# Kernel optimization log

Measured on AMD Instinct MI355X. Metric: run time of the kernel, lower is better.

Reference implementation:

```python
import jax, jax.numpy as jnp
import numpy as np
from jax import lax

EPS = 1e-5

def _layernorm(x, w, b):
    m = jnp.mean(x, axis=-1, keepdims=True)
    v = jnp.mean(jnp.square(x - m), axis=-1, keepdims=True)
    return (x - m) * lax.rsqrt(v + EPS) * w + b

def setup_inputs() -> dict:
    D = 2048
    B, S = 4, 4096
    key = jax.random.key(0)
    ks = jax.random.split(key, 16)
    f32 = jnp.float32
    inp = {
        "x": jax.random.normal(ks[0], (B, S, D), f32),
        "norm1_w": jnp.ones((D,), f32), "norm1_b": jnp.zeros((D,), f32),
        "norm2_w": jnp.ones((D,), f32), "norm2_b": jnp.zeros((D,), f32),
        "time_decay": jax.random.normal(ks[1], (D,), f32) * 0.01 - 5.0,
        "time_faaaa": jax.random.normal(ks[2], (D,), f32) * 0.01,
        # Linear weights stored as [in, out]; y = x @ W (equiv to torch x @ W.T)
        "Wr": jax.random.normal(ks[3], (D, D), f32) * 0.02,
        "Wk": jax.random.normal(ks[4], (D, D), f32) * 0.02,
        "Wv": jax.random.normal(ks[5], (D, D), f32) * 0.02,
        "Wo": jax.random.normal(ks[6], (D, D), f32) * 0.02,
        "time_mix_r": jnp.full((1, 1, D), 0.5, f32),
        "time_mix_k": jnp.full((1, 1, D), 0.5, f32),
        "time_mix_v": jnp.full((1, 1, D), 0.5, f32),
        "Wcr": jax.random.normal(ks[7], (D, D), f32) * 0.02,
        "Wck": jax.random.normal(ks[8], (D, 3 * D), f32) * 0.02,
        "Wcv": jax.random.normal(ks[9], (3 * D, D), f32) * 0.02,
        "cm_mix": jnp.full((1, 1, D), 0.5, f32),
    }
    return inp

def _wkv(r, k, v, time_decay, time_faaaa):
    # Elementwise linear recurrence: state_t = state_{t-1} * w + k_t * v_t
    w = jnp.exp(-jnp.exp(time_decay))            # [D]
    r_sig = jax.nn.sigmoid(r)                    # [B,S,D]
    kv = k * v                                   # [B,S,D]
    def step(state, kv_t):
        state = state * w + kv_t
        return state, state
    _, states = lax.scan(step, jnp.zeros_like(kv[:, 0]), jnp.swapaxes(kv, 0, 1))
    states = jnp.swapaxes(states, 0, 1)          # [B,S,D]
    out = r_sig * states
    # bonus only applies at t == 0 in the original loop
    out = out.at[:, 0].add(r_sig[:, 0] * jnp.exp(time_faaaa) * kv[:, 0])
    return out

def reference(x, norm1_w, norm1_b, norm2_w, norm2_b, time_decay, time_faaaa,
              Wr, Wk, Wv, Wo, time_mix_r, time_mix_k, time_mix_v,
              Wcr, Wck, Wcv, cm_mix):
    # time-mixing
    h = _layernorm(x, norm1_w, norm1_b)
    prev = jnp.pad(h[:, :-1], ((0, 0), (1, 0), (0, 0)))
    r = (h * time_mix_r + prev * (1.0 - time_mix_r)) @ Wr
    k = (h * time_mix_k + prev * (1.0 - time_mix_k)) @ Wk
    v = (h * time_mix_v + prev * (1.0 - time_mix_v)) @ Wv
    wkv = _wkv(r, k, v, time_decay, time_faaaa)
    x = x + wkv @ Wo
    # channel-mixing
    h = _layernorm(x, norm2_w, norm2_b)
    prev = jnp.pad(h[:, :-1], ((0, 0), (1, 0), (0, 0)))
    mixed = h * cm_mix + prev * (1.0 - cm_mix)
    r_cm = jax.nn.sigmoid(mixed @ Wcr)
    k_cm = jax.nn.relu(jnp.square(mixed @ Wck))
    x = x + r_cm * (k_cm @ Wcv)
    return x
```

## Files before the change

### kernel.cpp

```cpp
#include <hip/hip_runtime.h>
#include <stdint.h>
#include <stddef.h>


typedef float  f32x4   __attribute__((ext_vector_type(4)));
typedef short  short8  __attribute__((ext_vector_type(8)));
typedef short  short4_ __attribute__((ext_vector_type(4)));
typedef __bf16 bf16x8  __attribute__((ext_vector_type(8)));

constexpr int kD   = 2048;
constexpr int kSeq = 4096;
constexpr int kBat = 4;
constexpr int kM   = kBat * kSeq;
constexpr int kL   = 64;
constexpr int kC   = kSeq / kL;

__device__ __forceinline__ short f2bf(float f) {
  unsigned u = __builtin_bit_cast(unsigned, f);
  u += 0x7FFFu + ((u >> 16) & 1u);
  return (short)(u >> 16);
}
__device__ __forceinline__ float bf2f(short h) {
  unsigned u = ((unsigned)(unsigned short)h) << 16;
  return __builtin_bit_cast(float, u);
}
__device__ __forceinline__ void split_bf(float v, short& hi, short& lo) {
  hi = f2bf(v);
  lo = f2bf(v - bf2f(hi));
}

__device__ __forceinline__ f32x4 block_reduce4(f32x4 v) {
  #pragma unroll
  for (int off = 32; off > 0; off >>= 1) {
    v[0] += __shfl_down(v[0], off);
    v[1] += __shfl_down(v[1], off);
    v[2] += __shfl_down(v[2], off);
    v[3] += __shfl_down(v[3], off);
  }
  __shared__ float sh[4][4];
  const int wid = threadIdx.x >> 6, lane = threadIdx.x & 63;
  if (lane == 0) { sh[wid][0] = v[0]; sh[wid][1] = v[1]; sh[wid][2] = v[2]; sh[wid][3] = v[3]; }
  __syncthreads();
  #pragma unroll
  for (int i = 0; i < 4; ++i) v[i] = sh[0][i] + sh[1][i] + sh[2][i] + sh[3][i];
  return v;
}

__global__ __launch_bounds__(256) void wconvert_kernel(
    const float* __restrict__ W, short* __restrict__ hi, short* __restrict__ lo,
    int K, int N) {
  __shared__ float tile[32][33];
  const int tx = threadIdx.x & 31, ty = threadIdx.x >> 5;
  const int n0 = blockIdx.x * 32, k0 = blockIdx.y * 32;
  #pragma unroll
  for (int i = 0; i < 32; i += 8)
    tile[ty + i][tx] = W[(size_t)(k0 + ty + i) * N + (n0 + tx)];
  __syncthreads();
  #pragma unroll
  for (int i = 0; i < 32; i += 8) {
    float v = tile[tx][ty + i];
    int n = n0 + ty + i, k = k0 + tx;
    short h, l; split_bf(v, h, l);
    hi[(size_t)n * K + k] = h;
    lo[(size_t)n * K + k] = l;
  }
}

__global__ __launch_bounds__(256) void ln1mix_kernel(
    const float* __restrict__ x, const float* __restrict__ w1, const float* __restrict__ b1,
    const float* __restrict__ tmr, const float* __restrict__ tmk, const float* __restrict__ tmv,
    short* __restrict__ mr_hi, short* __restrict__ mr_lo,
    short* __restrict__ mk_hi, short* __restrict__ mk_lo,
    short* __restrict__ mv_hi, short* __restrict__ mv_lo) {
  const int row = blockIdx.x;
  const int s = row & (kSeq - 1);
  const float* xs = x + (size_t)row * kD;
  const int t = threadIdx.x;
  f32x4 a[2];
  f32x4 p[2] = {};
  a[0] = *(const f32x4*)&xs[4 * t];
  a[1] = *(const f32x4*)&xs[1024 + 4 * t];
  if (s > 0) {
    p[0] = *(const f32x4*)&xs[4 * t - kD];
    p[1] = *(const f32x4*)&xs[1024 + 4 * t - kD];
  }
  f32x4 sums = {0.f, 0.f, 0.f, 0.f};
  #pragma unroll
  for (int g = 0; g < 2; ++g)
    #pragma unroll
    for (int j = 0; j < 4; ++j) {
      sums[0] += a[g][j]; sums[1] += a[g][j] * a[g][j];
      sums[2] += p[g][j]; sums[3] += p[g][j] * p[g][j];
    }
  sums = block_reduce4(sums);
  const float inv = 1.f / kD;
  const float ms = sums[0] * inv, vs = sums[1] * inv - ms * ms;
  const float mp = sums[2] * inv, vp = sums[3] * inv - mp * mp;
  const float rs = rsqrtf(vs + 1e-5f);
  const float rp = rsqrtf(vp + 1e-5f);
  #pragma unroll
  for (int g = 0; g < 2; ++g) {
    const int d0 = g * 1024 + 4 * t;
    short4_ rh, rl, kh, kl, vh, vl;
    #pragma unroll
    for (int j = 0; j < 4; ++j) {
      const int d = d0 + j;
      const float w = w1[d], bb = b1[d];
      const float h  = (a[g][j] - ms) * rs * w + bb;
      const float hp = (s > 0) ? (p[g][j] - mp) * rp * w + bb : 0.f;
      const float cr = tmr[d], ck = tmk[d], cv = tmv[d];
      short th, tl;
      split_bf(h * cr + hp * (1.f - cr), th, tl); rh[j] = th; rl[j] = tl;
      split_bf(h * ck + hp * (1.f - ck), th, tl); kh[j] = th; kl[j] = tl;
      split_bf(h * cv + hp * (1.f - cv), th, tl); vh[j] = th; vl[j] = tl;
    }
    const size_t o = (size_t)row * kD + d0;
    *(short4_*)&mr_hi[o] = rh; *(short4_*)&mr_lo[o] = rl;
    *(short4_*)&mk_hi[o] = kh; *(short4_*)&mk_lo[o] = kl;
    *(short4_*)&mv_hi[o] = vh; *(short4_*)&mv_lo[o] = vl;
  }
}

__global__ __launch_bounds__(256) void lnmix_kernel(
    const float* __restrict__ xb, const float* __restrict__ w, const float* __restrict__ b,
    const float* __restrict__ coeff,
    short* __restrict__ mhi, short* __restrict__ mlo) {
  const int row = blockIdx.x;
  const int s = row & (kSeq - 1);
  const float* xs = xb + (size_t)row * kD;
  const int t = threadIdx.x;
  f32x4 a[2];
  f32x4 p[2] = {};
  a[0] = *(const f32x4*)&xs[4 * t];
  a[1] = *(const f32x4*)&xs[1024 + 4 * t];
  if (s > 0) {
    p[0] = *(const f32x4*)&xs[4 * t - kD];
    p[1] = *(const f32x4*)&xs[1024 + 4 * t - kD];
  }
  f32x4 sums = {0.f, 0.f, 0.f, 0.f};
  #pragma unroll
  for (int g = 0; g < 2; ++g)
    #pragma unroll
    for (int j = 0; j < 4; ++j) {
      sums[0] += a[g][j]; sums[1] += a[g][j] * a[g][j];
      sums[2] += p[g][j]; sums[3] += p[g][j] * p[g][j];
    }
  sums = block_reduce4(sums);
  const float inv = 1.f / kD;
  const float ms = sums[0] * inv, vs = sums[1] * inv - ms * ms;
  const float mp = sums[2] * inv, vp = sums[3] * inv - mp * mp;
  const float rs = rsqrtf(vs + 1e-5f);
  const float rp = rsqrtf(vp + 1e-5f);
  #pragma unroll
  for (int g = 0; g < 2; ++g) {
    const int d0 = g * 1024 + 4 * t;
    short4_ mh, ml;
    #pragma unroll
    for (int j = 0; j < 4; ++j) {
      const int d = d0 + j;
      const float ww = w[d], bb = b[d];
      const float h  = (a[g][j] - ms) * rs * ww + bb;
      const float hp = (s > 0) ? (p[g][j] - mp) * rp * ww + bb : 0.f;
      const float c = coeff[d];
      short th, tl;
      split_bf(h * c + hp * (1.f - c), th, tl);
      mh[j] = th; ml[j] = tl;
    }
    const size_t o = (size_t)row * kD + d0;
    *(short4_*)&mhi[o] = mh; *(short4_*)&mlo[o] = ml;
  }
}

__global__ __launch_bounds__(256) void scan1_kernel(
    const float* __restrict__ kv, const float* __restrict__ td,
    float* __restrict__ chunk_end) {
  const int idx = blockIdx.x * 256 + threadIdx.x;
  const int d = idx & (kD - 1);
  const int c = (idx >> 11) & (kC - 1);
  const int b = idx >> 17;
  const float w = expf(-expf(td[d]));
  const float* p = kv + ((size_t)b * kSeq + (size_t)c * kL) * kD + d;
  float st = 0.f;
  #pragma unroll 4
  for (int i = 0; i < kL; ++i) st = st * w + p[(size_t)i * kD];
  chunk_end[idx] = st;
}

__global__ __launch_bounds__(256) void scan2_kernel(
    const float* __restrict__ chunk_end, const float* __restrict__ td,
    float* __restrict__ carry) {
  const int idx = blockIdx.x * 256 + threadIdx.x;
  const int d = idx & (kD - 1);
  const int b = idx >> 11;
  const float wL = expf(-expf(td[d]) * (float)kL);
  float c = 0.f;
  for (int i = 0; i < kC; ++i) {
    const size_t o = ((size_t)b * kC + i) * kD + d;
    carry[o] = c;
    c = c * wL + chunk_end[o];
  }
}

__global__ __launch_bounds__(256) void scan3_kernel(
    const float* __restrict__ kv, const float* __restrict__ carry,
    const float* __restrict__ rsig, const float* __restrict__ td,
    const float* __restrict__ tf,
    short* __restrict__ whi, short* __restrict__ wlo) {
  const int idx = blockIdx.x * 256 + threadIdx.x;
  const int d = idx & (kD - 1);
  const int c = (idx >> 11) & (kC - 1);
  const int b = idx >> 17;
  const float w = expf(-expf(td[d]));
  float st = carry[idx];
  const size_t base = ((size_t)b * kSeq + (size_t)c * kL) * kD + d;
  const float bonus = (c == 0) ? expf(tf[d]) : 0.f;
  #pragma unroll 4
  for (int i = 0; i < kL; ++i) {
    const size_t o = base + (size_t)i * kD;
    const float kvv = kv[o];
    st = st * w + kvv;
    float out = rsig[o] * st;
    if (c == 0 && i == 0) out += rsig[o] * bonus * kvv;
    short h, l; split_bf(out, h, l);
    whi[o] = h; wlo[o] = l;
  }
}

constexpr int EPI_SIG = 0, EPI_NONE = 1, EPI_MULK = 2, EPI_ADDX = 3,
              EPI_SQ = 4, EPI_ACC0 = 5, EPI_ACC1 = 6, EPI_FINAL = 7;

#define AS1 __attribute__((address_space(1)))
#define AS3 __attribute__((address_space(3)))

template <int EPI>
__global__ __launch_bounds__(512, 2) void gemm256_kernel(
    const short* __restrict__ Ahi, const short* __restrict__ Alo,
    const short* __restrict__ Bhi, const short* __restrict__ Blo,
    int M, int N, int K, int ldb,
    float* __restrict__ outF,
    const float* __restrict__ aux1, const float* __restrict__ aux2,
    short* __restrict__ outHi, short* __restrict__ outLo) {
  __shared__ __align__(16) short As[2][256 * 64];
  __shared__ __align__(16) short Bs[2][256 * 64];
  const int tid = threadIdx.x;
  const int lane = tid & 63, wid = tid >> 6;
  const int wr = wid >> 2, wc = wid & 3;

  const int nwg = gridDim.x * gridDim.y;
  const int bid = blockIdx.y * gridDim.x + blockIdx.x;
  const int sw  = (bid & 7) * (nwg >> 3) + (bid >> 3);
  const int mBase = (sw / gridDim.x) * 256;
  const int nBase = (sw % gridDim.x) * 256;

  const int srow = lane >> 3;
  const int sgr  = (lane & 7) ^ srow;
  const int tpt  = K >> 6;
  const int ktiles = 3 * tpt;

  const int frow = lane & 15;
  const int quad = lane >> 4;

  f32x4 acc[8][4] = {};

  auto STAGE = [&](int t) {
    const int buf = t & 1;
    const int third = t / tpt;
    const int kk = (t - third * tpt) << 6;
    const short* __restrict__ Ab = (third == 1) ? Alo : Ahi;
    const short* __restrict__ Bb = (third == 2) ? Blo : Bhi;
    const int r0 = wid * 32;
    #pragma unroll
    for (int i = 0; i < 4; ++i) {
      const int rr = r0 + i * 8;
      const short* g = Ab + (size_t)(mBase + rr + srow) * K + kk + sgr * 8;
      __builtin_amdgcn_global_load_lds(
          (const AS1 void*)g, (AS3 void*)&As[buf][rr * 64], 16, 0, 0);
    }
    #pragma unroll
    for (int i = 0; i < 4; ++i) {
      const int rr = r0 + i * 8;
      const short* g = Bb + (size_t)(nBase + rr + srow) * ldb + kk + sgr * 8;
      __builtin_amdgcn_global_load_lds(
          (const AS1 void*)g, (AS3 void*)&Bs[buf][rr * 64], 16, 0, 0);
    }
  };

  STAGE(0);
  STAGE(1);

  for (int t = 0; t < ktiles; ++t) {
    const int buf = t & 1;
    if (t + 1 < ktiles) asm volatile("s_waitcnt vmcnt(8)");
    else                asm volatile("s_waitcnt vmcnt(0)");
    __builtin_amdgcn_s_barrier();
    asm volatile("" ::: "memory");

    short8 bfr[4][2];
    #pragma unroll
    for (int ni = 0; ni < 4; ++ni)
      #pragma unroll
      for (int ks = 0; ks < 2; ++ks) {
        const int row = wc * 64 + ni * 16 + frow;
        const int g = ks * 4 + quad;
        bfr[ni][ks] = *(const short8*)&Bs[buf][row * 64 + ((g ^ (row & 7)) << 3)];
      }

    #pragma unroll
    for (int p = 0; p < 4; ++p) {
      short8 afr[2][2];
      #pragma unroll
      for (int j = 0; j < 2; ++j)
        #pragma unroll
        for (int ks = 0; ks < 2; ++ks) {
          const int row = wr * 128 + (2 * p + j) * 16 + frow;
          const int g = ks * 4 + quad;
          afr[j][ks] = *(const short8*)&As[buf][row * 64 + ((g ^ (row & 7)) << 3)];
        }
      asm volatile("" ::: "memory");
      __builtin_amdgcn_s_barrier();
      asm volatile("s_waitcnt lgkmcnt(0)");
      __builtin_amdgcn_sched_barrier(0);
      __builtin_amdgcn_s_setprio(1);
      #pragma unroll
      for (int j = 0; j < 2; ++j)
        #pragma unroll
        for (int ni = 0; ni < 4; ++ni)
          #pragma unroll
          for (int ks = 0; ks < 2; ++ks)
            acc[2 * p + j][ni] = __builtin_amdgcn_mfma_f32_16x16x32_bf16(
                __builtin_bit_cast(bf16x8, afr[j][ks]),
                __builtin_bit_cast(bf16x8, bfr[ni][ks]),
                acc[2 * p + j][ni], 0, 0, 0);
      __builtin_amdgcn_s_setprio(0);
      __builtin_amdgcn_sched_barrier(0);
      asm volatile("" ::: "memory");
      __builtin_amdgcn_s_barrier();
    }
    if (t + 2 < ktiles) STAGE(t + 2);
  }

  #pragma unroll
  for (int mi = 0; mi < 8; ++mi) {
    #pragma unroll
    for (int ni = 0; ni < 4; ++ni) {
      const int gn = nBase + wc * 64 + ni * 16 + frow;
      #pragma unroll
      for (int r = 0; r < 4; ++r) {
        const int gm = mBase + wr * 128 + mi * 16 + quad * 4 + r;
        const size_t idx = (size_t)gm * N + gn;
        const float v = acc[mi][ni][r];
        if constexpr (EPI == EPI_SIG) {
          outF[idx] = 1.f / (1.f + expf(-v));
        } else if constexpr (EPI == EPI_NONE) {
          outF[idx] = v;
        } else if constexpr (EPI == EPI_MULK) {
          outF[idx] = v * aux1[idx];
        } else if constexpr (EPI == EPI_ADDX) {
          outF[idx] = v + aux1[idx];
        } else if constexpr (EPI == EPI_SQ) {
          const float q = v * v;
          short h, l; split_bf(q, h, l);
          outHi[idx] = h; outLo[idx] = l;
        } else if constexpr (EPI == EPI_ACC0) {
          outF[idx] = v;
        } else if constexpr (EPI == EPI_ACC1) {
          outF[idx] += v;
        } else {
          outF[idx] = aux1[idx] + aux2[idx] * (outF[idx] + v);
        }
      }
    }
  }
}

extern "C" void kernel_launch(void* const* d_in, const int* in_sizes, int n_in,
                              void* d_out, int out_size, void* d_ws, size_t ws_size,
                              hipStream_t stream) {
  const float* x   = (const float*)d_in[0];
  const float* n1w = (const float*)d_in[1];
  const float* n1b = (const float*)d_in[2];
  const float* n2w = (const float*)d_in[3];
  const float* n2b = (const float*)d_in[4];
  const float* td  = (const float*)d_in[5];
  const float* tf  = (const float*)d_in[6];
  const float* Wr  = (const float*)d_in[7];
  const float* Wk  = (const float*)d_in[8];
  const float* Wv  = (const float*)d_in[9];
  const float* Wo  = (const float*)d_in[10];
  const float* tmr = (const float*)d_in[11];
  const float* tmk = (const float*)d_in[12];
  const float* tmv = (const float*)d_in[13];
  const float* Wcr = (const float*)d_in[14];
  const float* Wck = (const float*)d_in[15];
  const float* Wcv = (const float*)d_in[16];
  const float* cm  = (const float*)d_in[17];
  float* out = (float*)d_out;

  const size_t D2 = (size_t)kD * kD;
  const size_t D3 = (size_t)kD * (3 * kD);
  const size_t wbytes = (10 * D2 + 4 * D3) * sizeof(short);

  auto need = [&](int nc_) -> size_t {
    const size_t Mc_ = (size_t)kM / nc_;
    const size_t scanb = 2 * ((size_t)(kBat / nc_) * kC * kD) * sizeof(float);
    return wbytes + scanb + 4 * (Mc_ * kD * sizeof(float));
  };
  int nc = 4;
  if (ws_size >= need(1)) nc = 1;
  else if (ws_size >= need(2)) nc = 2;

  const size_t Mc = (size_t)kM / nc;
  const int Bc = kBat / nc;

  short* wp = (short*)d_ws;
  short* WrT_hi  = wp; wp += D2;  short* WrT_lo  = wp; wp += D2;
  short* WkT_hi  = wp; wp += D2;  short* WkT_lo  = wp; wp += D2;
  short* WvT_hi  = wp; wp += D2;  short* WvT_lo  = wp; wp += D2;
  short* WoT_hi  = wp; wp += D2;  short* WoT_lo  = wp; wp += D2;
  short* WcrT_hi = wp; wp += D2;  short* WcrT_lo = wp; wp += D2;
  short* WckT_hi = wp; wp += D3;  short* WckT_lo = wp; wp += D3;
  short* WcvT_hi = wp; wp += D3;  short* WcvT_lo = wp; wp += D3;
  float* chunk_end = (float*)wp;
  float* carry = chunk_end + (size_t)Bc * kC * kD;
  float* slotA = carry + (size_t)Bc * kC * kD;
  float* slotB = slotA + Mc * kD;
  float* slotC = slotB + Mc * kD;
  float* slotD = slotC + Mc * kD;

  const dim3 blk(256);
  const dim3 gblk(512);

  wconvert_kernel<<<dim3(kD / 32, kD / 32), blk, 0, stream>>>(Wr,  WrT_hi,  WrT_lo,  kD, kD);
  wconvert_kernel<<<dim3(kD / 32, kD / 32), blk, 0, stream>>>(Wk,  WkT_hi,  WkT_lo,  kD, kD);
  wconvert_kernel<<<dim3(kD / 32, kD / 32), blk, 0, stream>>>(Wv,  WvT_hi,  WvT_lo,  kD, kD);
  wconvert_kernel<<<dim3(kD / 32, kD / 32), blk, 0, stream>>>(Wo,  WoT_hi,  WoT_lo,  kD, kD);
  wconvert_kernel<<<dim3(kD / 32, kD / 32), blk, 0, stream>>>(Wcr, WcrT_hi, WcrT_lo, kD, kD);
  wconvert_kernel<<<dim3(3 * kD / 32, kD / 32), blk, 0, stream>>>(Wck, WckT_hi, WckT_lo, kD, 3 * kD);
  wconvert_kernel<<<dim3(kD / 32, 3 * kD / 32), blk, 0, stream>>>(Wcv, WcvT_hi, WcvT_lo, 3 * kD, kD);

  for (int c = 0; c < nc; ++c) {
    const float* xc = x + (size_t)c * Mc * kD;
    float* outc = out + (size_t)c * Mc * kD;

    short* mr_hi = (short*)slotA; short* mr_lo = mr_hi + Mc * kD;
    short* mk_hi = (short*)slotB; short* mk_lo = mk_hi + Mc * kD;
    short* mv_hi = (short*)slotC; short* mv_lo = mv_hi + Mc * kD;
    float* r_sig = slotD;
    float* kbuf  = slotA;
    float* kvbuf = slotB;
    short* wkv_hi = (short*)slotC; short* wkv_lo = wkv_hi + Mc * kD;
    float* x1 = slotA;
    short* m2_hi = (short*)slotD; short* m2_lo = m2_hi + Mc * kD;
    float* r_cm = slotB;
    short* kcm_hi = (short*)slotC; short* kcm_lo = kcm_hi + Mc * kD;

    const dim3 g256(kD / 256, Mc / 256);

    ln1mix_kernel<<<Mc, blk, 0, stream>>>(xc, n1w, n1b, tmr, tmk, tmv,
                                          mr_hi, mr_lo, mk_hi, mk_lo, mv_hi, mv_lo);

    gemm256_kernel<EPI_SIG><<<g256, gblk, 0, stream>>>(
        mr_hi, mr_lo, WrT_hi, WrT_lo, (int)Mc, kD, kD, kD,
        r_sig, nullptr, nullptr, nullptr, nullptr);
    gemm256_kernel<EPI_NONE><<<g256, gblk, 0, stream>>>(
        mk_hi, mk_lo, WkT_hi, WkT_lo, (int)Mc, kD, kD, kD,
        kbuf, nullptr, nullptr, nullptr, nullptr);
    gemm256_kernel<EPI_MULK><<<g256, gblk, 0, stream>>>(
        mv_hi, mv_lo, WvT_hi, WvT_lo, (int)Mc, kD, kD, kD,
        kvbuf, kbuf, nullptr, nullptr, nullptr);

    scan1_kernel<<<(Bc * kC * kD) / 256, blk, 0, stream>>>(kvbuf, td, chunk_end);
    scan2_kernel<<<(Bc * kD) / 256, blk, 0, stream>>>(chunk_end, td, carry);
    scan3_kernel<<<(Bc * kC * kD) / 256, blk, 0, stream>>>(kvbuf, carry, r_sig, td, tf,
                                                           wkv_hi, wkv_lo);

    gemm256_kernel<EPI_ADDX><<<g256, gblk, 0, stream>>>(
        wkv_hi, wkv_lo, WoT_hi, WoT_lo, (int)Mc, kD, kD, kD,
        x1, xc, nullptr, nullptr, nullptr);

    lnmix_kernel<<<Mc, blk, 0, stream>>>(x1, n2w, n2b, cm, m2_hi, m2_lo);
    gemm256_kernel<EPI_SIG><<<g256, gblk, 0, stream>>>(
        m2_hi, m2_lo, WcrT_hi, WcrT_lo, (int)Mc, kD, kD, kD,
        r_cm, nullptr, nullptr, nullptr, nullptr);

    for (int j = 0; j < 3; ++j) {
      gemm256_kernel<EPI_SQ><<<g256, gblk, 0, stream>>>(
          m2_hi, m2_lo, WckT_hi + (size_t)j * kD * kD, WckT_lo + (size_t)j * kD * kD,
          (int)Mc, kD, kD, kD, nullptr, nullptr, nullptr, kcm_hi, kcm_lo);
      if (j == 0)
        gemm256_kernel<EPI_ACC0><<<g256, gblk, 0, stream>>>(
            kcm_hi, kcm_lo, WcvT_hi + (size_t)j * kD, WcvT_lo + (size_t)j * kD,
            (int)Mc, kD, kD, 3 * kD, outc, nullptr, nullptr, nullptr, nullptr);
      else if (j == 1)
        gemm256_kernel<EPI_ACC1><<<g256, gblk, 0, stream>>>(
            kcm_hi, kcm_lo, WcvT_hi + (size_t)j * kD, WcvT_lo + (size_t)j * kD,
            (int)Mc, kD, kD, 3 * kD, outc, nullptr, nullptr, nullptr, nullptr);
      else
        gemm256_kernel<EPI_FINAL><<<g256, gblk, 0, stream>>>(
            kcm_hi, kcm_lo, WcvT_hi + (size_t)j * kD, WcvT_lo + (size_t)j * kD,
            (int)Mc, kD, kD, 3 * kD, outc, x1, r_cm, nullptr, nullptr);
    }
  }
}
```

Before: 5.971 ms.

## Interleave B-tile prefetch into MFMA sub-steps and relax GEMM launch bounds

The B-operand global-to-LDS staging for tile t+2 is split into two halves and issued during the p=1 and p=2 compute sub-steps, after the B fragments are already in registers. The A staging stays at the end of the iteration. This spreads memory issue across the compute loop instead of bursting it at the end. Launch bounds drop from 2 to 1 waves-per-EU hint, which frees register budget; with 128KB of LDS per block only one block fits per CU anyway. Several sched_barriers are also removed, which gives the compiler freedom to reorder but risks it interleaving LDS reads with MFMAs badly.

Measured after the change: 6.079 ms. About the same (+1.8%).

```diff
diff --git a/kernel.cpp b/kernel.cpp
--- a/kernel.cpp
+++ b/kernel.cpp
@@ -233,7 +233,7 @@
 #define AS3 __attribute__((address_space(3)))
 
 template <int EPI>
-__global__ __launch_bounds__(512, 2) void gemm256_kernel(
+__global__ __launch_bounds__(512, 1) void gemm256_kernel(
     const short* __restrict__ Ahi, const short* __restrict__ Alo,
     const short* __restrict__ Bhi, const short* __restrict__ Blo,
     int M, int N, int K, int ldb,
@@ -262,38 +262,47 @@
 
   f32x4 acc[8][4] = {};
 
-  auto STAGE = [&](int t) {
+  auto kkOf = [&](int t, const short*& Ab, const short*& Bb) -> int {
+    const int third = t / tpt;
+    Ab = (third == 1) ? Alo : Ahi;
+    Bb = (third == 2) ? Blo : Bhi;
+    return (t - third * tpt) << 6;
+  };
+
+  auto STAGE_A = [&](int t) {
+    const short *Ab, *Bb;
+    const int kk = kkOf(t, Ab, Bb);
     const int buf = t & 1;
-    const int third = t / tpt;
-    const int kk = (t - third * tpt) << 6;
-    const short* __restrict__ Ab = (third == 1) ? Alo : Ahi;
-    const short* __restrict__ Bb = (third == 2) ? Blo : Bhi;
-    const int r0 = wid * 32;
     #pragma unroll
     for (int i = 0; i < 4; ++i) {
-      const int rr = r0 + i * 8;
+      const int rr = wid * 32 + i * 8;
       const short* g = Ab + (size_t)(mBase + rr + srow) * K + kk + sgr * 8;
       __builtin_amdgcn_global_load_lds(
           (const AS1 void*)g, (AS3 void*)&As[buf][rr * 64], 16, 0, 0);
     }
-    #pragma unroll
-    for (int i = 0; i < 4; ++i) {
-      const int rr = r0 + i * 8;
+  };
+  auto STAGE_B = [&](int t, int half) {
+    const short *Ab, *Bb;
+    const int kk = kkOf(t, Ab, Bb);
+    const int buf = t & 1;
+    #pragma unroll
+    for (int i = 0; i < 2; ++i) {
+      const int rr = wid * 32 + (half * 2 + i) * 8;
       const short* g = Bb + (size_t)(nBase + rr + srow) * ldb + kk + sgr * 8;
       __builtin_amdgcn_global_load_lds(
           (const AS1 void*)g, (AS3 void*)&Bs[buf][rr * 64], 16, 0, 0);
     }
   };
 
-  STAGE(0);
-  STAGE(1);
+  STAGE_A(0); STAGE_B(0, 0); STAGE_B(0, 1);
+  STAGE_A(1); STAGE_B(1, 0); STAGE_B(1, 1);
 
   for (int t = 0; t < ktiles; ++t) {
     const int buf = t & 1;
     if (t + 1 < ktiles) asm volatile("s_waitcnt vmcnt(8)");
     else                asm volatile("s_waitcnt vmcnt(0)");
+    asm volatile("" ::: "memory");
     __builtin_amdgcn_s_barrier();
-    asm volatile("" ::: "memory");
 
     short8 bfr[4][2];
     #pragma unroll
@@ -316,10 +325,10 @@
           const int g = ks * 4 + quad;
           afr[j][ks] = *(const short8*)&As[buf][row * 64 + ((g ^ (row & 7)) << 3)];
         }
-      asm volatile("" ::: "memory");
+      if ((p == 1 || p == 2) && t + 2 < ktiles) STAGE_B(t + 2, p - 1);
+
       __builtin_amdgcn_s_barrier();
       asm volatile("s_waitcnt lgkmcnt(0)");
-      __builtin_amdgcn_sched_barrier(0);
       __builtin_amdgcn_s_setprio(1);
       #pragma unroll
       for (int j = 0; j < 2; ++j)
@@ -332,11 +341,9 @@
                 __builtin_bit_cast(bf16x8, bfr[ni][ks]),
                 acc[2 * p + j][ni], 0, 0, 0);
       __builtin_amdgcn_s_setprio(0);
-      __builtin_amdgcn_sched_barrier(0);
-      asm volatile("" ::: "memory");
       __builtin_amdgcn_s_barrier();
     }
-    if (t + 2 < ktiles) STAGE(t + 2);
+    if (t + 2 < ktiles) STAGE_A(t + 2);
   }
 
   #pragma unroll
```
